# Kernel tuning notes

Hardware: AMD Instinct MI355X
Metric: run time of the kernel (lower is better)

The kernel has to match this reference:

```python
import jax, jax.numpy as jnp
import numpy as np

NUM_NODES = 116
EMBED = 64
HIDDEN = 64
OUT_FEAT = 116


def mish(x):
    return x * jnp.tanh(jax.nn.softplus(x))


def sage_conv(x, src, dst, w_l, b_l, w_r, n):
    # PyG SAGEConv (mean aggr): out = lin_l(mean_{j->i} x_j) + lin_r(x_i)
    agg = jax.ops.segment_sum(x[src], dst, num_segments=n)
    cnt = jax.ops.segment_sum(jnp.ones((src.shape[0],), x.dtype), dst, num_segments=n)
    mean = agg / jnp.clip(cnt, 1.0)[:, None]
    return mean @ w_l.T + b_l + x @ w_r.T


def setup_inputs() -> dict:
    key = jax.random.key(0)
    ks = jax.random.split(key, 12)
    B = 64
    N = B * NUM_NODES          # 7424 total nodes
    E = N * 32                 # 237568 edges
    d_in = EMBED * NUM_NODES   # 7424
    d_hid = HIDDEN * NUM_NODES # 7424
    d_out = OUT_FEAT * NUM_NODES  # 13456

    def lin_w(k, fan_out, fan_in):
        s = 1.0 / np.sqrt(fan_in)
        return jax.random.uniform(k, (fan_out, fan_in), jnp.float32, -s, s)

    return {
        "z": jax.random.normal(ks[0], (N, EMBED), jnp.float32),
        "edge_index": jax.random.randint(ks[1], (2, E), 0, N, jnp.int64),
        "batch_size": B,
        "w1_l": lin_w(ks[2], EMBED, EMBED),
        "b1_l": jnp.zeros((EMBED,), jnp.float32),
        "w1_r": lin_w(ks[3], EMBED, EMBED),
        "w2_l": lin_w(ks[4], EMBED, EMBED),
        "b2_l": jnp.zeros((EMBED,), jnp.float32),
        "w2_r": lin_w(ks[5], EMBED, EMBED),
        "fc1_w": lin_w(ks[6], d_hid, d_in),
        "fc1_b": jax.random.uniform(ks[7], (d_hid,), jnp.float32, -1/np.sqrt(d_in), 1/np.sqrt(d_in)),
        "fc2_w": lin_w(ks[8], d_out, d_hid),
        "fc2_b": jax.random.uniform(ks[9], (d_out,), jnp.float32, -1/np.sqrt(d_hid), 1/np.sqrt(d_hid)),
    }


def reference(z, edge_index, batch_size, w1_l, b1_l, w1_r, w2_l, b2_l, w2_r,
              fc1_w, fc1_b, fc2_w, fc2_b):
    n = z.shape[0]
    src, dst = edge_index[0], edge_index[1]
    h = mish(sage_conv(z, src, dst, w1_l, b1_l, w1_r, n))
    h = mish(sage_conv(h, src, dst, w2_l, b2_l, w2_r, n))
    h_flat = h.reshape(batch_size, NUM_NODES * EMBED)
    hidden = mish(h_flat @ fc1_w.T + fc1_b)
    x_rec = (hidden @ fc2_w.T + fc2_b).reshape(batch_size, NUM_NODES, OUT_FEAT)
    # enforce symmetry, unit diagonal
    sym = 0.5 * (x_rec + jnp.swapaxes(x_rec, 1, 2))
    eye = jnp.eye(NUM_NODES, dtype=bool)[None]
    sym = jnp.where(eye, jnp.asarray(1.0, sym.dtype), sym)
    return sym.reshape(batch_size * NUM_NODES, OUT_FEAT)
```

## Files before the change

kernel.cpp:

```cpp
#include <hip/hip_runtime.h>
#include <math.h>

#define NODES_TOT 7424
#define EDGES     237568
#define BATCH     64
#define NN        116
#define KDIM      7424
#define N1        7424
#define N2        13456
#define NKB       116
#define KSPLIT1   8
#define KSPLIT2   4

typedef __attribute__((ext_vector_type(8))) short bf16x8;
typedef __attribute__((ext_vector_type(4))) float f32x4;
typedef __attribute__((ext_vector_type(4))) short s16x4;

__device__ __forceinline__ float mish_f(float v) {
    float sp = fmaxf(v, 0.0f) + log1pf(expf(-fabsf(v)));
    return v * tanhf(sp);
}

__device__ __forceinline__ unsigned short bf_rne(float f) {
    unsigned u = __float_as_uint(f);
    u += 0x7fffu + ((u >> 16) & 1u);
    return (unsigned short)(u >> 16);
}

__device__ __forceinline__ void gload_lds16(const void* g, void* l) {
    __builtin_amdgcn_global_load_lds(
        (const __attribute__((address_space(1))) void*)g,
        (__attribute__((address_space(3))) void*)l, 16, 0, 0);
}

__global__ void zero_kernel(int* __restrict__ p, int n) {
    int i = blockIdx.x * 256 + threadIdx.x;
    if (i < n) p[i] = 0;
}

__global__ void hist_kernel(const int* __restrict__ dst, int* __restrict__ hist) {
    int e = blockIdx.x * 256 + threadIdx.x;
    if (e < EDGES) atomicAdd(&hist[dst[e]], 1);
}

__global__ void scan_kernel(const int* __restrict__ hist, int* __restrict__ row_start,
                            int* __restrict__ cursor) {
    __shared__ int s[1024];
    int t = threadIdx.x;
    int base = t * 8;
    int loc[8];
    int sum = 0;
    #pragma unroll
    for (int c = 0; c < 8; ++c) {
        int idx = base + c;
        int v = (idx < NODES_TOT) ? hist[idx] : 0;
        loc[c] = sum;
        sum += v;
    }
    s[t] = sum;
    __syncthreads();
    for (int off = 1; off < 1024; off <<= 1) {
        int v = (t >= off) ? s[t - off] : 0;
        __syncthreads();
        s[t] += v;
        __syncthreads();
    }
    int excl = s[t] - sum;
    #pragma unroll
    for (int c = 0; c < 8; ++c) {
        int idx = base + c;
        if (idx < NODES_TOT) {
            int r = excl + loc[c];
            row_start[idx] = r;
            cursor[idx] = r;
        }
    }
}

__global__ void csr_fill_kernel(const int* __restrict__ src, const int* __restrict__ dst,
                                int* __restrict__ cursor, int* __restrict__ csr_src) {
    int e = blockIdx.x * 256 + threadIdx.x;
    if (e < EDGES) {
        int p = atomicAdd(&cursor[dst[e]], 1);
        csr_src[p] = src[e];
    }
}

template <bool BF>
__global__ void __launch_bounds__(256) conv_kernel(
        const float* __restrict__ x, const int* __restrict__ csr_src,
        const int* __restrict__ row_start, const int* __restrict__ deg_arr,
        const float* __restrict__ w_l, const float* __restrict__ b_l,
        const float* __restrict__ w_r, void* __restrict__ h_out_v) {
    __shared__ float wlT[64 * 64];
    __shared__ float wrT[64 * 64];
    __shared__ float mv[4][64];
    __shared__ float xv[4][64];
    int t = threadIdx.x;
    for (int i = 0; i < 16; ++i) {
        int idx = t + i * 256;
        int f = idx >> 6, k = idx & 63;
        wlT[k * 64 + f] = w_l[idx];
        wrT[k * 64 + f] = w_r[idx];
    }
    int g = t >> 6, f = t & 63;
    __syncthreads();
    for (int nb = blockIdx.x * 4; nb < NODES_TOT; nb += gridDim.x * 4) {
        int node = nb + g;
        int deg = deg_arr[node];
        int rs = row_start[node];
        float sum = 0.f;
        for (int e = 0; e < deg; ++e) {
            int s = csr_src[rs + e];
            sum += x[s * 64 + f];
        }
        float mean = sum / (float)max(deg, 1);
        mv[g][f] = mean;
        xv[g][f] = x[node * 64 + f];
        __syncthreads();
        float o = b_l[f];
        #pragma unroll
        for (int k = 0; k < 64; ++k) {
            o = fmaf(mv[g][k], wlT[k * 64 + f], o);
            o = fmaf(xv[g][k], wrT[k * 64 + f], o);
        }
        float m = mish_f(o);
        if (BF) ((unsigned short*)h_out_v)[node * 64 + f] = bf_rne(m);
        else    ((float*)h_out_v)[node * 64 + f] = m;
        __syncthreads();
    }
}

template <int KS>
__global__ void __launch_bounds__(256) gemm_dma(
        const unsigned short* __restrict__ Abf, const float* __restrict__ W,
        float* __restrict__ Cp, int N) {
    __shared__ __align__(16) float          Wlds[2][4096];
    __shared__ __align__(16) unsigned short Alds[2][4096];
    int t = threadIdx.x;
    int bx = blockIdx.x, by = blockIdx.y;
    int kb0 = (by * NKB) / KS;
    int kb1 = ((by + 1) * NKB) / KS;
    int S = kb1 - kb0;
    int n0 = bx * 64;
    int wv = t >> 6, l = t & 63, l15 = l & 15, hi = l >> 4;

    const float* wsrc[4];
    #pragma unroll
    for (int ii = 0; ii < 4; ++ii) {
        int rloc = wv * 16 + ii * 4 + (l >> 4);
        int wr = n0 + rloc; if (wr >= N) wr = N - 1;
        int g = (l & 15) ^ ((rloc & 7) << 1);
        wsrc[ii] = W + (size_t)wr * KDIM + (size_t)kb0 * 64 + g * 4;
    }
    const unsigned short* asrcp[2];
    #pragma unroll
    for (int ii = 0; ii < 2; ++ii) {
        int rloc = wv * 16 + ii * 8 + (l >> 3);
        int g = (l & 7) ^ (rloc & 7);
        asrcp[ii] = Abf + (size_t)rloc * KDIM + (size_t)kb0 * 64 + g * 8;
    }

    f32x4 acc[4];
    #pragma unroll
    for (int g = 0; g < 4; ++g) acc[g] = (f32x4){0.f, 0.f, 0.f, 0.f};

#define ISSUE(step, buf) do {                                              \
        size_t ko = (size_t)(step) * 64;                                   \
        _Pragma("unroll")                                                  \
        for (int ii = 0; ii < 4; ++ii)                                     \
            gload_lds16(wsrc[ii] + ko, &Wlds[buf][(wv * 16 + ii * 4) * 64]); \
        _Pragma("unroll")                                                  \
        for (int ii = 0; ii < 2; ++ii)                                     \
            gload_lds16(asrcp[ii] + ko, &Alds[buf][(wv * 16 + ii * 8) * 64]); \
    } while (0)

#define MFMAPH(buf) do {                                                   \
        _Pragma("unroll")                                                  \
        for (int s = 0; s < 2; ++s) {                                      \
            int fw = s * 4 + hi;                                           \
            int n = wv * 16 + l15;                                         \
            int g0 = (2 * fw) ^ ((n & 7) << 1);                            \
            f32x4 wlo = *(const f32x4*)&Wlds[buf][n * 64 + g0 * 4];        \
            f32x4 whi = *(const f32x4*)&Wlds[buf][n * 64 + g0 * 4 + 4];    \
            bf16x8 bh;                                                     \
            _Pragma("unroll")                                              \
            for (int j = 0; j < 4; ++j) {                                  \
                bh[j]     = (short)bf_rne(wlo[j]);                         \
                bh[4 + j] = (short)bf_rne(whi[j]);                         \
            }                                                              \
            _Pragma("unroll")                                              \
            for (int g = 0; g < 4; ++g) {                                  \
                int ar = g * 16 + l15;                                     \
                bf16x8 av = *(const bf16x8*)&Alds[buf][ar * 64 + ((fw ^ (ar & 7)) * 8)]; \
                acc[g] = __builtin_amdgcn_mfma_f32_16x16x32_bf16(av, bh, acc[g], 0, 0, 0); \
            }                                                              \
        }                                                                  \
    } while (0)

#define WAIT6()  asm volatile("s_waitcnt vmcnt(6)" ::: "memory")
#define WAIT0()  asm volatile("s_waitcnt vmcnt(0)" ::: "memory")
#define RBAR()   asm volatile("s_barrier" ::: "memory")
#define LBAR()   asm volatile("s_waitcnt lgkmcnt(0)\n\ts_barrier" ::: "memory")

    ISSUE(0, 0);
    ISSUE(1, 1);
    WAIT6();
    RBAR();

    int i = 0;
    while (true) {
        MFMAPH(0);
        LBAR();
        if (i + 2 < S) { ISSUE(i + 2, 0); WAIT6(); } else { WAIT0(); }
        RBAR();
        if (++i == S) break;
        MFMAPH(1);
        LBAR();
        if (i + 2 < S) { ISSUE(i + 2, 1); WAIT6(); } else { WAIT0(); }
        RBAR();
        if (++i == S) break;
    }

#undef ISSUE
#undef MFMAPH
#undef WAIT6
#undef WAIT0
#undef RBAR
#undef LBAR

    int gn = n0 + wv * 16 + l15;
    if (gn < N) {
        float* cp = Cp + (size_t)by * 64 * N;
        #pragma unroll
        for (int g = 0; g < 4; ++g)
            #pragma unroll
            for (int rr = 0; rr < 4; ++rr)
                cp[(size_t)(g * 16 + hi * 4 + rr) * N + gn] = acc[g][rr];
    }
}

__global__ void reduce1_kernel(const float* __restrict__ Cp, const float* __restrict__ b,
                               unsigned short* __restrict__ A2) {
    int i4 = (blockIdx.x * 256 + threadIdx.x) * 4;
    if (i4 >= BATCH * N1) return;
    int n = i4 % N1;
    f32x4 acc = *(const f32x4*)(b + n);
    #pragma unroll
    for (int s = 0; s < KSPLIT1; ++s)
        acc += *(const f32x4*)(Cp + (size_t)s * BATCH * N1 + i4);
    s16x4 o;
    #pragma unroll
    for (int j = 0; j < 4; ++j) o[j] = (short)bf_rne(mish_f(acc[j]));
    *(s16x4*)(A2 + i4) = o;
}

__global__ void reduce2_kernel(const float* __restrict__ Cp, const float* __restrict__ b,
                               float* __restrict__ C2) {
    int i4 = (blockIdx.x * 256 + threadIdx.x) * 4;
    if (i4 >= BATCH * N2) return;
    int n = i4 % N2;
    f32x4 acc = *(const f32x4*)(b + n);
    #pragma unroll
    for (int s = 0; s < KSPLIT2; ++s)
        acc += *(const f32x4*)(Cp + (size_t)s * BATCH * N2 + i4);
    *(f32x4*)(C2 + i4) = acc;
}

__global__ void sym_kernel(const float* __restrict__ C2, float* __restrict__ out) {
    int tid = blockIdx.x * 256 + threadIdx.x;
    if (tid >= BATCH * NN * NN) return;
    int j = tid % NN;
    int r = tid / NN;
    int i = r % NN;
    int b = r / NN;
    float v;
    if (i == j) {
        v = 1.0f;
    } else {
        v = 0.5f * (C2[(size_t)b * N2 + i * NN + j] + C2[(size_t)b * N2 + j * NN + i]);
    }
    out[tid] = v;
}

extern "C" void kernel_launch(void* const* d_in, const int* in_sizes, int n_in,
                              void* d_out, int out_size, void* d_ws, size_t ws_size,
                              hipStream_t stream) {
    const float* z     = (const float*)d_in[0];
    const int*   edge  = (const int*)d_in[1];
    const float* w1_l  = (const float*)d_in[3];
    const float* b1_l  = (const float*)d_in[4];
    const float* w1_r  = (const float*)d_in[5];
    const float* w2_l  = (const float*)d_in[6];
    const float* b2_l  = (const float*)d_in[7];
    const float* w2_r  = (const float*)d_in[8];
    const float* fc1_w = (const float*)d_in[9];
    const float* fc1_b = (const float*)d_in[10];
    const float* fc2_w = (const float*)d_in[11];
    const float* fc2_b = (const float*)d_in[12];
    float* out = (float*)d_out;

    char* ws = (char*)d_ws;
    size_t off = 0;
    auto alloc = [&](size_t bytes) {
        void* p = ws + off;
        off = (off + bytes + 255) & ~(size_t)255;
        return p;
    };
    int*            hist      = (int*)alloc(NODES_TOT * 4);
    int*            row_start = (int*)alloc(NODES_TOT * 4);
    int*            cursor    = (int*)alloc(NODES_TOT * 4);
    int*            csr_src   = (int*)alloc((size_t)EDGES * 4);
    float*          h1        = (float*)alloc((size_t)NODES_TOT * 64 * 4);
    unsigned short* A1        = (unsigned short*)alloc((size_t)NODES_TOT * 64 * 2);
    float*          Cp1       = (float*)alloc((size_t)KSPLIT1 * BATCH * N1 * 4);
    unsigned short* A2        = (unsigned short*)alloc((size_t)BATCH * N1 * 2);
    float*          Cp2       = (float*)alloc((size_t)KSPLIT2 * BATCH * N2 * 4);
    float*          C2        = (float*)alloc((size_t)BATCH * N2 * 4);

    const int* src = edge;
    const int* dst = edge + EDGES;

    zero_kernel<<<(NODES_TOT + 255) / 256, 256, 0, stream>>>(hist, NODES_TOT);
    hist_kernel<<<(EDGES + 255) / 256, 256, 0, stream>>>(dst, hist);
    scan_kernel<<<1, 1024, 0, stream>>>(hist, row_start, cursor);
    csr_fill_kernel<<<(EDGES + 255) / 256, 256, 0, stream>>>(src, dst, cursor, csr_src);

    conv_kernel<false><<<928, 256, 0, stream>>>(z, csr_src, row_start, hist, w1_l, b1_l, w1_r, h1);
    conv_kernel<true><<<928, 256, 0, stream>>>(h1, csr_src, row_start, hist, w2_l, b2_l, w2_r, A1);

    gemm_dma<KSPLIT1><<<dim3(N1 / 64, KSPLIT1), 256, 0, stream>>>(A1, fc1_w, Cp1, N1);
    reduce1_kernel<<<(BATCH * N1 / 4 + 255) / 256, 256, 0, stream>>>(Cp1, fc1_b, A2);

    gemm_dma<KSPLIT2><<<dim3((N2 + 63) / 64, KSPLIT2), 256, 0, stream>>>(A2, fc2_w, Cp2, N2);
    reduce2_kernel<<<(BATCH * N2 / 4 + 255) / 256, 256, 0, stream>>>(Cp2, fc2_b, C2);

    sym_kernel<<<(BATCH * NN * NN + 255) / 256, 256, 0, stream>>>(C2, out);
}
```

Before: 333.5 us.

## Use triple-buffered LDS ring in split-K GEMMs and unify K-split to 8

The split-K GEMM goes from a double-buffered LDS pipeline to a three-stage ring, so two tiles' global-to-LDS DMA loads are in flight while one tile is consumed by MFMA. The wait counts are adjusted per stage. The second GEMM's K-split also rises from 4 to 8, giving more blocks, at the cost of larger partial-sum buffers and more reduction reads. LDS use per block grows by half (about 72KB), which may lower occupancy.

```diff
diff --git a/kernel.cpp b/kernel.cpp
--- a/kernel.cpp
+++ b/kernel.cpp
@@ -9,8 +9,7 @@
 #define N1        7424
 #define N2        13456
 #define NKB       116
-#define KSPLIT1   8
-#define KSPLIT2   4
+#define KSPLIT    8
 
 typedef __attribute__((ext_vector_type(8))) short bf16x8;
 typedef __attribute__((ext_vector_type(4))) float f32x4;
@@ -132,11 +131,11 @@
 }
 
 template <int KS>
-__global__ void __launch_bounds__(256) gemm_dma(
+__global__ void __launch_bounds__(256) gemm_ring(
         const unsigned short* __restrict__ Abf, const float* __restrict__ W,
         float* __restrict__ Cp, int N) {
-    __shared__ __align__(16) float          Wlds[2][4096];
-    __shared__ __align__(16) unsigned short Alds[2][4096];
+    __shared__ __align__(16) float          Wlds[3][4096];
+    __shared__ __align__(16) unsigned short Alds[3][4096];
     int t = threadIdx.x;
     int bx = blockIdx.x, by = blockIdx.y;
     int kb0 = (by * NKB) / KS;
@@ -198,6 +197,7 @@
         }                                                                  \
     } while (0)
 
+#define WAIT12() asm volatile("s_waitcnt vmcnt(12)" ::: "memory")
 #define WAIT6()  asm volatile("s_waitcnt vmcnt(6)" ::: "memory")
 #define WAIT0()  asm volatile("s_waitcnt vmcnt(0)" ::: "memory")
 #define RBAR()   asm volatile("s_barrier" ::: "memory")
@@ -205,25 +205,23 @@
 
     ISSUE(0, 0);
     ISSUE(1, 1);
-    WAIT6();
-    RBAR();
-
-    int i = 0;
-    while (true) {
-        MFMAPH(0);
+    ISSUE(2, 2);
+
+    int b = 0;
+    for (int s = 0; s < S; ++s) {
+        if (s < S - 2) WAIT12();
+        else if (s == S - 2) WAIT6();
+        else WAIT0();
+        RBAR();
+        MFMAPH(b);
         LBAR();
-        if (i + 2 < S) { ISSUE(i + 2, 0); WAIT6(); } else { WAIT0(); }
-        RBAR();
-        if (++i == S) break;
-        MFMAPH(1);
-        LBAR();
-        if (i + 2 < S) { ISSUE(i + 2, 1); WAIT6(); } else { WAIT0(); }
-        RBAR();
-        if (++i == S) break;
+        if (s + 3 < S) ISSUE(s + 3, b);
+        b = (b == 2) ? 0 : b + 1;
     }
 
 #undef ISSUE
 #undef MFMAPH
+#undef WAIT12
 #undef WAIT6
 #undef WAIT0
 #undef RBAR
@@ -247,7 +245,7 @@
     int n = i4 % N1;
     f32x4 acc = *(const f32x4*)(b + n);
     #pragma unroll
-    for (int s = 0; s < KSPLIT1; ++s)
+    for (int s = 0; s < KSPLIT; ++s)
         acc += *(const f32x4*)(Cp + (size_t)s * BATCH * N1 + i4);
     s16x4 o;
     #pragma unroll
@@ -262,7 +260,7 @@
     int n = i4 % N2;
     f32x4 acc = *(const f32x4*)(b + n);
     #pragma unroll
-    for (int s = 0; s < KSPLIT2; ++s)
+    for (int s = 0; s < KSPLIT; ++s)
         acc += *(const f32x4*)(Cp + (size_t)s * BATCH * N2 + i4);
     *(f32x4*)(C2 + i4) = acc;
 }
@@ -313,9 +311,9 @@
     int*            csr_src   = (int*)alloc((size_t)EDGES * 4);
     float*          h1        = (float*)alloc((size_t)NODES_TOT * 64 * 4);
     unsigned short* A1        = (unsigned short*)alloc((size_t)NODES_TOT * 64 * 2);
-    float*          Cp1       = (float*)alloc((size_t)KSPLIT1 * BATCH * N1 * 4);
+    float*          Cp1       = (float*)alloc((size_t)KSPLIT * BATCH * N1 * 4);
     unsigned short* A2        = (unsigned short*)alloc((size_t)BATCH * N1 * 2);
-    float*          Cp2       = (float*)alloc((size_t)KSPLIT2 * BATCH * N2 * 4);
+    float*          Cp2       = (float*)alloc((size_t)KSPLIT * BATCH * N2 * 4);
     float*          C2        = (float*)alloc((size_t)BATCH * N2 * 4);
 
     const int* src = edge;
@@ -329,10 +327,10 @@
     conv_kernel<false><<<928, 256, 0, stream>>>(z, csr_src, row_start, hist, w1_l, b1_l, w1_r, h1);
     conv_kernel<true><<<928, 256, 0, stream>>>(h1, csr_src, row_start, hist, w2_l, b2_l, w2_r, A1);
 
-    gemm_dma<KSPLIT1><<<dim3(N1 / 64, KSPLIT1), 256, 0, stream>>>(A1, fc1_w, Cp1, N1);
+    gemm_ring<KSPLIT><<<dim3(N1 / 64, KSPLIT), 256, 0, stream>>>(A1, fc1_w, Cp1, N1);
     reduce1_kernel<<<(BATCH * N1 / 4 + 255) / 256, 256, 0, stream>>>(Cp1, fc1_b, A2);
 
-    gemm_dma<KSPLIT2><<<dim3((N2 + 63) / 64, KSPLIT2), 256, 0, stream>>>(A2, fc2_w, Cp2, N2);
+    gemm_ring<KSPLIT><<<dim3((N2 + 63) / 64, KSPLIT), 256, 0, stream>>>(A2, fc2_w, Cp2, N2);
     reduce2_kernel<<<(BATCH * N2 / 4 + 255) / 256, 256, 0, stream>>>(Cp2, fc2_b, C2);
 
     sym_kernel<<<(BATCH * NN * NN + 255) / 256, 256, 0, stream>>>(C2, out);
```

Measured after the change: 332.0 us. About the same (-0.4%).
